# Optimization experiments

Hardware: AMD Instinct MI355X
Metric: run time of the kernel (lower is better)

The kernel has to match this reference:

```python
import jax, jax.numpy as jnp
import numpy as np

NUM_LAYERS = 5
EMB_DIM = 300
NUM_ATOM_TYPE = 121
NUM_CHIRALITY = 11
NUM_BOND_TYPE = 7
NUM_BOND_DIR = 3
BN_EPS = 1e-5


def setup_inputs() -> dict:
    key = jax.random.key(0)
    ks = jax.random.split(key, 16)
    N, E, D, L = 100000, 200000, EMB_DIM, NUM_LAYERS

    def glorot(k, shape):
        fan_in, fan_out = shape[-2], shape[-1]
        s = jnp.sqrt(6.0 / (fan_in + fan_out))
        return jax.random.uniform(k, shape, jnp.float32, -s, s)

    x = jax.random.randint(ks[0], (N, 2), 0, 11)  # atom type / chirality (both < 11, in range)
    edge_index = jax.random.randint(ks[1], (2, E), 0, N)
    edge_attr = jax.random.randint(ks[2], (E, 2), 0, 3)

    return {
        "x": x,
        "edge_index": edge_index,
        "edge_attr": edge_attr,
        "x_emb1": glorot(ks[3], (NUM_ATOM_TYPE, D)),
        "x_emb2": glorot(ks[4], (NUM_CHIRALITY, D)),
        "edge_emb1": glorot(ks[5], (L, NUM_BOND_TYPE, D)),
        "edge_emb2": glorot(ks[6], (L, NUM_BOND_DIR, D)),
        "w1": glorot(ks[7], (L, D, 2 * D)),
        "b1": jnp.zeros((L, 2 * D), jnp.float32),
        "w2": glorot(ks[8], (L, 2 * D, D)),
        "b2": jnp.zeros((L, D), jnp.float32),
        "bn_gamma": jnp.ones((L, D), jnp.float32),
        "bn_beta": jnp.zeros((L, D), jnp.float32),
    }


def reference(x, edge_index, edge_attr, x_emb1, x_emb2, edge_emb1, edge_emb2,
              w1, b1, w2, b2, bn_gamma, bn_beta):
    N = x.shape[0]
    # GINConv.forward adds self loops with edge_attr row [4, 0]
    loop = jnp.arange(N)
    src = jnp.concatenate([edge_index[0], loop])  # [E+N]
    dst = jnp.concatenate([edge_index[1], loop])  # [E+N]
    ea0 = jnp.concatenate([edge_attr[:, 0], jnp.full((N,), 4, edge_attr.dtype)])
    ea1 = jnp.concatenate([edge_attr[:, 1], jnp.zeros((N,), edge_attr.dtype)])

    # node input embedding
    h = x_emb1[x[:, 0]] + x_emb2[x[:, 1]]  # [N, D]

    for l in range(NUM_LAYERS):
        # edge embeddings (incl. self loops)
        eemb = edge_emb1[l][ea0] + edge_emb2[l][ea1]  # [E+N, D]
        # message: x_j + edge_attr, aggr='add' at destination nodes
        msg = h[src] + eemb
        agg = jax.ops.segment_sum(msg, dst, num_segments=N)  # [N, D]
        # GIN update MLP: Linear(D, 2D) -> ReLU -> Linear(2D, D)
        h2 = jax.nn.relu(agg @ w1[l] + b1[l]) @ w2[l] + b2[l]
        # BatchNorm1d (training mode: batch statistics, biased variance)
        mean = h2.mean(axis=0)
        var = h2.var(axis=0)
        h2 = (h2 - mean) * jax.lax.rsqrt(var + BN_EPS) * bn_gamma[l] + bn_beta[l]
        # ReLU on all but last layer (dropout is identity, drop_ratio=0)
        if l < NUM_LAYERS - 1:
            h2 = jax.nn.relu(h2)
        h = h2
    # JK == 'last'
    return h
```

## Files before the change

kernel.cpp:

```cpp
#include <hip/hip_runtime.h>
#include <hip/hip_bf16.h>
#include <stdint.h>

typedef __bf16 bf16_t;
typedef bf16_t bf16x8 __attribute__((ext_vector_type(8)));
typedef float  f32x4  __attribute__((ext_vector_type(4)));

__device__ __forceinline__ void g2l16(const void* gp, void* lp) {
  __builtin_amdgcn_global_load_lds(
      (const __attribute__((address_space(1))) unsigned int*)(uintptr_t)gp,
      (__attribute__((address_space(3))) unsigned int*)(uint32_t)(uintptr_t)lp,
      16, 0, 0);
}

__global__ void embed_kernel(const int* __restrict__ x, const float* __restrict__ e1,
                             const float* __restrict__ e2, bf16_t* __restrict__ h, int N) {
  const int w = (blockIdx.x * blockDim.x + threadIdx.x) >> 6;
  const int lane = threadIdx.x & 63;
  if (w >= N || lane >= 40) return;
  const int t0 = x[2 * w], t1 = x[2 * w + 1];
  const int co = lane * 8;
  f32x4 a0 = *(const f32x4*)&e1[t0 * 300 + co];
  f32x4 a1 = *(const f32x4*)&e1[t0 * 300 + co + 4];
  f32x4 b0 = *(const f32x4*)&e2[t1 * 300 + co];
  f32x4 b1 = *(const f32x4*)&e2[t1 * 300 + co + 4];
  bf16x8 o;
  #pragma unroll
  for (int j = 0; j < 8; j++) {
    float v = (j < 4) ? (a0[j] + b0[j]) : (a1[j - 4] + b1[j - 4]);
    o[j] = (co + j < 300) ? (bf16_t)v : (bf16_t)0.f;
  }
  *(bf16x8*)&h[(size_t)w * 320 + co] = o;
}

__global__ void count_deg_kernel(const int* __restrict__ ei, int* __restrict__ deg, int E) {
  int e = blockIdx.x * 256 + threadIdx.x;
  if (e < E) atomicAdd(&deg[ei[E + e]], 1);
}

__global__ void scan_partial_kernel(const int* __restrict__ deg, int* __restrict__ part, int N) {
  __shared__ int s[256];
  const int tid = threadIdx.x;
  const int idx = blockIdx.x * 256 + tid;
  s[tid] = (idx < N) ? deg[idx] : 0;
  __syncthreads();
  for (int off = 128; off > 0; off >>= 1) {
    if (tid < off) s[tid] += s[tid + off];
    __syncthreads();
  }
  if (tid == 0) part[blockIdx.x] = s[0];
}

__global__ void scan_block_kernel(int* __restrict__ part, int n) {
  __shared__ int s[1024];
  const int tid = threadIdx.x;
  const int v = (tid < n) ? part[tid] : 0;
  s[tid] = v;
  __syncthreads();
  for (int off = 1; off < 1024; off <<= 1) {
    int x = (tid >= off) ? s[tid - off] : 0;
    __syncthreads();
    s[tid] += x;
    __syncthreads();
  }
  if (tid < n) part[tid] = s[tid] - v;
}

__global__ void scan_final_kernel(const int* __restrict__ deg, const int* __restrict__ part,
                                  int* __restrict__ rowptr, int* __restrict__ cursor, int N, int E) {
  __shared__ int s[256];
  const int tid = threadIdx.x;
  const int idx = blockIdx.x * 256 + tid;
  const int v = (idx < N) ? deg[idx] : 0;
  s[tid] = v;
  __syncthreads();
  for (int off = 1; off < 256; off <<= 1) {
    int x = (tid >= off) ? s[tid - off] : 0;
    __syncthreads();
    s[tid] += x;
    __syncthreads();
  }
  if (idx < N) {
    int ex = s[tid] - v + part[blockIdx.x];
    rowptr[idx] = ex;
    cursor[idx] = ex;
  }
  if (idx == 0) rowptr[N] = E;
}

__global__ void fill_csr_kernel(const int* __restrict__ ei, const int* __restrict__ ea,
                                int* __restrict__ cursor, int* __restrict__ epack, int E) {
  int e = blockIdx.x * 256 + threadIdx.x;
  if (e >= E) return;
  int slot = atomicAdd(&cursor[ei[E + e]], 1);
  int a = ea[2 * e] * 3 + ea[2 * e + 1];
  epack[slot] = (ei[e] & 0xFFFFF) | (a << 20);
}

__global__ void convert_w1_kernel(const float* __restrict__ w1, bf16_t* __restrict__ o) {
  int id = blockIdx.x * 256 + threadIdx.x;
  if (id >= 5 * 640 * 320) return;
  int k = id % 320;
  int n = (id / 320) % 640;
  int l = id / (320 * 640);
  float v = (k < 300 && n < 600) ? w1[(size_t)l * 300 * 600 + (size_t)k * 600 + n] : 0.f;
  o[id] = (bf16_t)v;
}

__global__ void convert_w2_kernel(const float* __restrict__ w2, bf16_t* __restrict__ o) {
  int id = blockIdx.x * 256 + threadIdx.x;
  if (id >= 5 * 384 * 640) return;
  int k = id % 640;
  int n = (id / 640) % 384;
  int l = id / (640 * 384);
  float v = (k < 600 && n < 300) ? w2[(size_t)l * 600 * 300 + (size_t)k * 300 + n] : 0.f;
  o[id] = (bf16_t)v;
}

__global__ void build_t12_kernel(const float* __restrict__ ee1, const float* __restrict__ ee2,
                                 bf16_t* __restrict__ T12) {
  int id = blockIdx.x * 256 + threadIdx.x;
  if (id >= 5 * 21 * 320) return;
  int col = id % 320;
  int r = id / 320;
  int l = r / 21;
  int a = r % 21;
  int a0 = a / 3, a1 = a % 3;
  float v = 0.f;
  if (col < 300) v = ee1[((size_t)l * 7 + a0) * 300 + col] + ee2[((size_t)l * 3 + a1) * 300 + col];
  T12[id] = (bf16_t)v;
}

__global__ void aggregate_kernel(const bf16_t* __restrict__ h, const int* __restrict__ rowptr,
                                 const int* __restrict__ epack, const bf16_t* __restrict__ T12L,
                                 bf16_t* __restrict__ agg, int N) {
  const int w = (blockIdx.x * blockDim.x + threadIdx.x) >> 6;
  const int lane = threadIdx.x & 63;
  if (w >= N || lane >= 40) return;
  const int co = lane * 8;
  const int beg = rowptr[w], end = rowptr[w + 1];
  float acc[8];
  {
    bf16x8 hv = *(const bf16x8*)&h[(size_t)w * 320 + co];
    bf16x8 tv = *(const bf16x8*)&T12L[12 * 320 + co];
    #pragma unroll
    for (int j = 0; j < 8; j++) acc[j] = (float)hv[j] + (float)tv[j];
  }
  for (int e = beg; e < end; e++) {
    const int p = epack[e];
    const int s = p & 0xFFFFF;
    const int a = (p >> 20) & 0x1F;
    bf16x8 hv = *(const bf16x8*)&h[(size_t)s * 320 + co];
    bf16x8 tv = *(const bf16x8*)&T12L[a * 320 + co];
    #pragma unroll
    for (int j = 0; j < 8; j++) acc[j] += (float)hv[j] + (float)tv[j];
  }
  bf16x8 o;
  #pragma unroll
  for (int j = 0; j < 8; j++) o[j] = (bf16_t)acc[j];
  *(bf16x8*)&agg[(size_t)w * 320 + co] = o;
}

template <int LDA, int LDB, int LDC, int NK, int GY, int NBIAS, bool RELU, bool STATS>
__global__ __launch_bounds__(256) void gemm_kernel(const bf16_t* __restrict__ A,
                                                   const bf16_t* __restrict__ BT,
                                                   const float* __restrict__ bias,
                                                   bf16_t* __restrict__ C,
                                                   float* __restrict__ sums,
                                                   float* __restrict__ sumsq,
                                                   int Nvalid, int nwg) {
  __shared__ __align__(16) bf16_t As0[128 * 32];
  __shared__ __align__(16) bf16_t Bs0[128 * 32];
  __shared__ __align__(16) bf16_t As1[128 * 32];
  __shared__ __align__(16) bf16_t Bs1[128 * 32];

  const int tid = threadIdx.x;
  const int lane = tid & 63;
  const int wave = tid >> 6;
  const int ml = lane & 15, quad = lane >> 4;
  const int wm = (wave & 1) * 64, wn = (wave >> 1) * 64;
  const int kx = ml & 3;

  const int bid = blockIdx.x;
  const int q = nwg >> 3, r = nwg & 7;
  const int xcd = bid & 7, pos = bid >> 3;
  const int logical = (xcd < r ? xcd * (q + 1) : r * (q + 1) + (xcd - r) * q) + pos;
  const size_t bm = (size_t)(logical / GY) * 128;
  const size_t bnn = (size_t)(logical % GY) * 128;

  const int srow = tid >> 2;
  const int cg = (tid & 3) ^ (srow & 3);
  const bf16_t* ag = A + (bm + srow) * LDA + cg * 8;
  const bf16_t* bg = BT + (bnn + srow) * LDB + cg * 8;

  auto stage = [&](bf16_t* as, bf16_t* bs, int kb) {
    const int kof = kb * 32;
    #pragma unroll
    for (int it = 0; it < 2; it++) {
      g2l16(ag + (size_t)it * 64 * LDA + kof, (void*)&as[((size_t)it * 256 + tid) * 8]);
      g2l16(bg + (size_t)it * 64 * LDB + kof, (void*)&bs[((size_t)it * 256 + tid) * 8]);
    }
  };

  f32x4 acc[4][4];
  #pragma unroll
  for (int rr = 0; rr < 4; rr++)
    #pragma unroll
    for (int cc = 0; cc < 4; cc++) acc[rr][cc] = (f32x4){0.f, 0.f, 0.f, 0.f};

  auto compute = [&](const bf16_t* as, const bf16_t* bs) {
    const int ck = quad ^ kx;
    bf16x8 aF[4], bF[4];
    #pragma unroll
    for (int mf = 0; mf < 4; mf++)
      aF[mf] = *(const bf16x8*)&as[((wm + mf * 16 + ml) * 4 + ck) * 8];
    #pragma unroll
    for (int nf = 0; nf < 4; nf++)
      bF[nf] = *(const bf16x8*)&bs[((wn + nf * 16 + ml) * 4 + ck) * 8];
    #pragma unroll
    for (int mf = 0; mf < 4; mf++)
      #pragma unroll
      for (int nf = 0; nf < 4; nf++)
        acc[mf][nf] = __builtin_amdgcn_mfma_f32_16x16x32_bf16(aF[mf], bF[nf], acc[mf][nf], 0, 0, 0);
  };

  stage(As0, Bs0, 0);
  __syncthreads();

  #pragma unroll 2
  for (int kp = 0; kp < NK / 2; kp++) {
    stage(As1, Bs1, 2 * kp + 1);
    compute(As0, Bs0);
    __syncthreads();
    if (kp + 1 < NK / 2) stage(As0, Bs0, 2 * kp + 2);
    compute(As1, Bs1);
    __syncthreads();
  }

  #pragma unroll
  for (int nf = 0; nf < 4; nf++) {
    const int colg = (int)bnn + wn + nf * 16 + ml;
    const float bv = (colg < NBIAS) ? bias[colg] : 0.f;
    float s = 0.f, sq = 0.f;
    #pragma unroll
    for (int mf = 0; mf < 4; mf++) {
      #pragma unroll
      for (int i = 0; i < 4; i++) {
        const size_t rowg = bm + wm + mf * 16 + quad * 4 + i;
        float v = acc[mf][nf][i] + bv;
        if (RELU) v = fmaxf(v, 0.f);
        C[rowg * LDC + colg] = (bf16_t)v;
        if (STATS) {
          const bool ok = rowg < (size_t)Nvalid;
          s += ok ? v : 0.f;
          sq += ok ? v * v : 0.f;
        }
      }
    }
    if (STATS) {
      s += __shfl_down(s, 16);
      sq += __shfl_down(sq, 16);
      s += __shfl_down(s, 32);
      sq += __shfl_down(sq, 32);
      if (quad == 0) {
        atomicAdd(&sums[colg], s);
        atomicAdd(&sumsq[colg], sq);
      }
    }
  }
}

__global__ void bn_params_kernel(const float* __restrict__ sums, const float* __restrict__ sumsq,
                                 const float* __restrict__ gamma, const float* __restrict__ beta,
                                 float* __restrict__ scale, float* __restrict__ shift, int N) {
  const int col = threadIdx.x;
  if (col >= 384) return;
  if (col >= 300) {
    scale[col] = 0.f;
    shift[col] = 0.f;
    return;
  }
  const float inv = 1.f / (float)N;
  const float mean = sums[col] * inv;
  float var = sumsq[col] * inv - mean * mean;
  if (var < 0.f) var = 0.f;
  const float sc = gamma[col] * rsqrtf(var + 1e-5f);
  scale[col] = sc;
  shift[col] = beta[col] - mean * sc;
}

__global__ void bn_apply_kernel(const bf16_t* __restrict__ H2, const float* __restrict__ scale,
                                const float* __restrict__ shift, bf16_t* __restrict__ h,
                                float* __restrict__ out, int relu, int last, int N) {
  const int w = (blockIdx.x * blockDim.x + threadIdx.x) >> 6;
  const int lane = threadIdx.x & 63;
  if (w >= N || lane >= 40) return;
  const int co = lane * 8;
  bf16x8 v8 = *(const bf16x8*)&H2[(size_t)w * 384 + co];
  f32x4 s0 = *(const f32x4*)&scale[co];
  f32x4 s1 = *(const f32x4*)&scale[co + 4];
  f32x4 t0 = *(const f32x4*)&shift[co];
  f32x4 t1 = *(const f32x4*)&shift[co + 4];
  float vv[8];
  #pragma unroll
  for (int j = 0; j < 8; j++) {
    float sc = (j < 4) ? s0[j] : s1[j - 4];
    float sh = (j < 4) ? t0[j] : t1[j - 4];
    float v = (float)v8[j] * sc + sh;
    if (relu) v = fmaxf(v, 0.f);
    vv[j] = v;
  }
  if (!last) {
    bf16x8 o;
    #pragma unroll
    for (int j = 0; j < 8; j++) o[j] = (bf16_t)vv[j];
    *(bf16x8*)&h[(size_t)w * 320 + co] = o;
  } else {
    #pragma unroll
    for (int j = 0; j < 8; j++)
      if (co + j < 300) out[(size_t)w * 300 + co + j] = vv[j];
  }
}

extern "C" void kernel_launch(void* const* d_in, const int* in_sizes, int n_in,
                              void* d_out, int out_size, void* d_ws, size_t ws_size,
                              hipStream_t stream) {
  const int* x = (const int*)d_in[0];
  const int* ei = (const int*)d_in[1];
  const int* ea = (const int*)d_in[2];
  const float* xe1 = (const float*)d_in[3];
  const float* xe2 = (const float*)d_in[4];
  const float* ee1 = (const float*)d_in[5];
  const float* ee2 = (const float*)d_in[6];
  const float* w1 = (const float*)d_in[7];
  const float* b1 = (const float*)d_in[8];
  const float* w2 = (const float*)d_in[9];
  const float* b2 = (const float*)d_in[10];
  const float* gam = (const float*)d_in[11];
  const float* bet = (const float*)d_in[12];

  const int N = in_sizes[0] / 2;
  const int E = in_sizes[1] / 2;
  const int Mt = (N + 127) / 128;
  const size_t Mp = (size_t)Mt * 128;

  char* p = (char*)d_ws;
  auto take = [&](size_t b) -> char* {
    char* r = p;
    p += (b + 255) & ~(size_t)255;
    return r;
  };
  bf16_t* h    = (bf16_t*)take(Mp * 320 * 2);
  bf16_t* agg  = (bf16_t*)take(Mp * 320 * 2);
  bf16_t* C1   = (bf16_t*)take(Mp * 640 * 2);
  bf16_t* H2   = (bf16_t*)take(Mp * 384 * 2);
  bf16_t* W1bT = (bf16_t*)take((size_t)5 * 640 * 320 * 2);
  bf16_t* W2bT = (bf16_t*)take((size_t)5 * 384 * 640 * 2);
  bf16_t* T12  = (bf16_t*)take((size_t)5 * 21 * 320 * 2);
  int* deg     = (int*)take((size_t)N * 4);
  int* rowptr  = (int*)take((size_t)(N + 1) * 4);
  int* cursor  = (int*)take((size_t)N * 4);
  int* part    = (int*)take(1024 * 4);
  int* epack   = (int*)take((size_t)E * 4);
  float* sums  = (float*)take(384 * 4);
  float* sumsq = (float*)take(384 * 4);
  float* scale = (float*)take(384 * 4);
  float* shift = (float*)take(384 * 4);

  hipMemsetAsync(agg, 0, Mp * 320 * 2, stream);
  hipMemsetAsync(deg, 0, (size_t)N * 4, stream);

  const int nwb = (N + 3) / 4;
  embed_kernel<<<nwb, 256, 0, stream>>>(x, xe1, xe2, h, N);

  count_deg_kernel<<<(E + 255) / 256, 256, 0, stream>>>(ei, deg, E);
  const int nsb = (N + 255) / 256;
  scan_partial_kernel<<<nsb, 256, 0, stream>>>(deg, part, N);
  scan_block_kernel<<<1, 1024, 0, stream>>>(part, nsb);
  scan_final_kernel<<<nsb, 256, 0, stream>>>(deg, part, rowptr, cursor, N, E);
  fill_csr_kernel<<<(E + 255) / 256, 256, 0, stream>>>(ei, ea, cursor, epack, E);

  convert_w1_kernel<<<(5 * 640 * 320 + 255) / 256, 256, 0, stream>>>(w1, W1bT);
  convert_w2_kernel<<<(5 * 384 * 640 + 255) / 256, 256, 0, stream>>>(w2, W2bT);
  build_t12_kernel<<<(5 * 21 * 320 + 255) / 256, 256, 0, stream>>>(ee1, ee2, T12);

  const int nwg1 = Mt * 5;
  const int nwg2 = Mt * 3;

  for (int l = 0; l < 5; l++) {
    aggregate_kernel<<<nwb, 256, 0, stream>>>(h, rowptr, epack, T12 + (size_t)l * 21 * 320,
                                              agg, N);
    gemm_kernel<320, 320, 640, 10, 5, 600, true, false>
        <<<nwg1, 256, 0, stream>>>(agg, W1bT + (size_t)l * 640 * 320,
                                   b1 + (size_t)l * 600, C1, sums, sumsq, N, nwg1);
    hipMemsetAsync(sums, 0, 384 * 4, stream);
    hipMemsetAsync(sumsq, 0, 384 * 4, stream);
    gemm_kernel<640, 640, 384, 20, 3, 300, false, true>
        <<<nwg2, 256, 0, stream>>>(C1, W2bT + (size_t)l * 384 * 640,
                                   b2 + (size_t)l * 300, H2, sums, sumsq, N, nwg2);
    bn_params_kernel<<<1, 384, 0, stream>>>(sums, sumsq, gam + (size_t)l * 300,
                                            bet + (size_t)l * 300, scale, shift, N);
    bn_apply_kernel<<<nwb, 256, 0, stream>>>(H2, scale, shift, h, (float*)d_out,
                                             (l < 4) ? 1 : 0, (l == 4) ? 1 : 0, N);
  }
}
```

Measured before the change: 1.621 ms.

## Fuse BN+ReLU into aggregation gather and triple-buffer GEMM K pipeline

Removes the per-layer bn_apply pass by applying the batch-norm scale/shift and ReLU on the fly while gathering neighbour rows from H2 inside the aggregation kernel. Only the final layer still runs a separate apply. The aggregation kernel now packs 40 lanes per node densely instead of wasting 24 of 64 lanes. The GEMM moves from double to triple buffering with explicit vmcnt waits and a changed LDS swizzle, which allows deeper load/compute overlap at the cost of more LDS per block. The fused path recomputes the BN math once per edge rather than once per node.

```diff
diff --git a/kernel.cpp b/kernel.cpp
--- a/kernel.cpp
+++ b/kernel.cpp
@@ -131,29 +131,50 @@
   T12[id] = (bf16_t)v;
 }
 
-__global__ void aggregate_kernel(const bf16_t* __restrict__ h, const int* __restrict__ rowptr,
+template <bool FUSE_BN>
+__global__ void aggregate_kernel(const bf16_t* __restrict__ hsrc, const int* __restrict__ rowptr,
                                  const int* __restrict__ epack, const bf16_t* __restrict__ T12L,
-                                 bf16_t* __restrict__ agg, int N) {
-  const int w = (blockIdx.x * blockDim.x + threadIdx.x) >> 6;
-  const int lane = threadIdx.x & 63;
-  if (w >= N || lane >= 40) return;
-  const int co = lane * 8;
+                                 const float* __restrict__ scale, const float* __restrict__ shift,
+                                 bf16_t* __restrict__ agg, int N, int LDH) {
+  const int g = blockIdx.x * 256 + threadIdx.x;
+  const int w = g / 40;
+  if (w >= N) return;
+  const int co = (g - w * 40) * 8;
+
+  float sc[8], sh[8];
+  if (FUSE_BN) {
+    f32x4 s0 = *(const f32x4*)&scale[co];
+    f32x4 s1 = *(const f32x4*)&scale[co + 4];
+    f32x4 t0 = *(const f32x4*)&shift[co];
+    f32x4 t1 = *(const f32x4*)&shift[co + 4];
+    #pragma unroll
+    for (int j = 0; j < 4; j++) { sc[j] = s0[j]; sc[j + 4] = s1[j]; sh[j] = t0[j]; sh[j + 4] = t1[j]; }
+  }
+
   const int beg = rowptr[w], end = rowptr[w + 1];
   float acc[8];
   {
-    bf16x8 hv = *(const bf16x8*)&h[(size_t)w * 320 + co];
+    bf16x8 hv = *(const bf16x8*)&hsrc[(size_t)w * LDH + co];
     bf16x8 tv = *(const bf16x8*)&T12L[12 * 320 + co];
     #pragma unroll
-    for (int j = 0; j < 8; j++) acc[j] = (float)hv[j] + (float)tv[j];
+    for (int j = 0; j < 8; j++) {
+      float v = (float)hv[j];
+      if (FUSE_BN) v = fmaxf(v * sc[j] + sh[j], 0.f);
+      acc[j] = v + (float)tv[j];
+    }
   }
   for (int e = beg; e < end; e++) {
     const int p = epack[e];
     const int s = p & 0xFFFFF;
     const int a = (p >> 20) & 0x1F;
-    bf16x8 hv = *(const bf16x8*)&h[(size_t)s * 320 + co];
+    bf16x8 hv = *(const bf16x8*)&hsrc[(size_t)s * LDH + co];
     bf16x8 tv = *(const bf16x8*)&T12L[a * 320 + co];
     #pragma unroll
-    for (int j = 0; j < 8; j++) acc[j] += (float)hv[j] + (float)tv[j];
+    for (int j = 0; j < 8; j++) {
+      float v = (float)hv[j];
+      if (FUSE_BN) v = fmaxf(v * sc[j] + sh[j], 0.f);
+      acc[j] += v + (float)tv[j];
+    }
   }
   bf16x8 o;
   #pragma unroll
@@ -173,13 +194,15 @@
   __shared__ __align__(16) bf16_t Bs0[128 * 32];
   __shared__ __align__(16) bf16_t As1[128 * 32];
   __shared__ __align__(16) bf16_t Bs1[128 * 32];
+  __shared__ __align__(16) bf16_t As2[128 * 32];
+  __shared__ __align__(16) bf16_t Bs2[128 * 32];
 
   const int tid = threadIdx.x;
   const int lane = tid & 63;
   const int wave = tid >> 6;
   const int ml = lane & 15, quad = lane >> 4;
   const int wm = (wave & 1) * 64, wn = (wave >> 1) * 64;
-  const int kx = ml & 3;
+  const int kx = (ml >> 1) & 3;
 
   const int bid = blockIdx.x;
   const int q = nwg >> 3, r = nwg & 7;
@@ -189,7 +212,7 @@
   const size_t bnn = (size_t)(logical % GY) * 128;
 
   const int srow = tid >> 2;
-  const int cg = (tid & 3) ^ (srow & 3);
+  const int cg = (tid & 3) ^ ((tid >> 3) & 3);
   const bf16_t* ag = A + (bm + srow) * LDA + cg * 8;
   const bf16_t* bg = BT + (bnn + srow) * LDB + cg * 8;
 
@@ -201,6 +224,8 @@
       g2l16(bg + (size_t)it * 64 * LDB + kof, (void*)&bs[((size_t)it * 256 + tid) * 8]);
     }
   };
+  auto bufA = [&](int i) -> bf16_t* { return i == 0 ? As0 : (i == 1 ? As1 : As2); };
+  auto bufB = [&](int i) -> bf16_t* { return i == 0 ? Bs0 : (i == 1 ? Bs1 : Bs2); };
 
   f32x4 acc[4][4];
   #pragma unroll
@@ -225,16 +250,23 @@
   };
 
   stage(As0, Bs0, 0);
-  __syncthreads();
-
-  #pragma unroll 2
-  for (int kp = 0; kp < NK / 2; kp++) {
-    stage(As1, Bs1, 2 * kp + 1);
-    compute(As0, Bs0);
-    __syncthreads();
-    if (kp + 1 < NK / 2) stage(As0, Bs0, 2 * kp + 2);
-    compute(As1, Bs1);
-    __syncthreads();
+  stage(As1, Bs1, 1);
+
+  #pragma unroll
+  for (int kb = 0; kb < NK; kb++) {
+    if (kb + 2 < NK) {
+      stage(bufA((kb + 2) % 3), bufB((kb + 2) % 3), kb + 2);
+      asm volatile("s_waitcnt vmcnt(8)" ::: "memory");
+    } else if (kb + 1 < NK) {
+      asm volatile("s_waitcnt vmcnt(4)" ::: "memory");
+    } else {
+      asm volatile("s_waitcnt vmcnt(0)" ::: "memory");
+    }
+    __builtin_amdgcn_s_barrier();
+    __builtin_amdgcn_sched_barrier(0);
+    compute(bufA(kb % 3), bufB(kb % 3));
+    __builtin_amdgcn_sched_barrier(0);
+    __builtin_amdgcn_s_barrier();
   }
 
   #pragma unroll
@@ -290,8 +322,7 @@
 }
 
 __global__ void bn_apply_kernel(const bf16_t* __restrict__ H2, const float* __restrict__ scale,
-                                const float* __restrict__ shift, bf16_t* __restrict__ h,
-                                float* __restrict__ out, int relu, int last, int N) {
+                                const float* __restrict__ shift, float* __restrict__ out, int N) {
   const int w = (blockIdx.x * blockDim.x + threadIdx.x) >> 6;
   const int lane = threadIdx.x & 63;
   if (w >= N || lane >= 40) return;
@@ -301,24 +332,12 @@
   f32x4 s1 = *(const f32x4*)&scale[co + 4];
   f32x4 t0 = *(const f32x4*)&shift[co];
   f32x4 t1 = *(const f32x4*)&shift[co + 4];
-  float vv[8];
   #pragma unroll
   for (int j = 0; j < 8; j++) {
     float sc = (j < 4) ? s0[j] : s1[j - 4];
     float sh = (j < 4) ? t0[j] : t1[j - 4];
     float v = (float)v8[j] * sc + sh;
-    if (relu) v = fmaxf(v, 0.f);
-    vv[j] = v;
-  }
-  if (!last) {
-    bf16x8 o;
-    #pragma unroll
-    for (int j = 0; j < 8; j++) o[j] = (bf16_t)vv[j];
-    *(bf16x8*)&h[(size_t)w * 320 + co] = o;
-  } else {
-    #pragma unroll
-    for (int j = 0; j < 8; j++)
-      if (co + j < 300) out[(size_t)w * 300 + co + j] = vv[j];
+    if (co + j < 300) out[(size_t)w * 300 + co + j] = v;
   }
 }
 
@@ -386,10 +405,18 @@
 
   const int nwg1 = Mt * 5;
   const int nwg2 = Mt * 3;
+  const int nab = (N * 40 + 255) / 256;
 
   for (int l = 0; l < 5; l++) {
-    aggregate_kernel<<<nwb, 256, 0, stream>>>(h, rowptr, epack, T12 + (size_t)l * 21 * 320,
-                                              agg, N);
+    if (l == 0) {
+      aggregate_kernel<false><<<nab, 256, 0, stream>>>(h, rowptr, epack,
+                                                       T12 + (size_t)l * 21 * 320,
+                                                       scale, shift, agg, N, 320);
+    } else {
+      aggregate_kernel<true><<<nab, 256, 0, stream>>>(H2, rowptr, epack,
+                                                      T12 + (size_t)l * 21 * 320,
+                                                      scale, shift, agg, N, 384);
+    }
     gemm_kernel<320, 320, 640, 10, 5, 600, true, false>
         <<<nwg1, 256, 0, stream>>>(agg, W1bT + (size_t)l * 640 * 320,
                                    b1 + (size_t)l * 600, C1, sums, sumsq, N, nwg1);
@@ -400,7 +427,6 @@
                                    b2 + (size_t)l * 300, H2, sums, sumsq, N, nwg2);
     bn_params_kernel<<<1, 384, 0, stream>>>(sums, sumsq, gam + (size_t)l * 300,
                                             bet + (size_t)l * 300, scale, shift, N);
-    bn_apply_kernel<<<nwb, 256, 0, stream>>>(H2, scale, shift, h, (float*)d_out,
-                                             (l < 4) ? 1 : 0, (l == 4) ? 1 : 0, N);
-  }
-}
+  }
+  bn_apply_kernel<<<nwb, 256, 0, stream>>>(H2, scale, shift, (float*)d_out, N);
+}
```

Result: faster. 1.367 ms (-15.6%).
